# Kernel optimization log

Measured on AMD Instinct MI355X. Metric: run time of the kernel, lower is better.

## Reference

```python
import jax, jax.numpy as jnp
import numpy as np

VAR = 1.0
STD = float(np.sqrt(VAR))


def setup_inputs() -> dict:
    key = jax.random.key(0)
    k1, k2 = jax.random.split(key)
    n, c = 262144, 100
    scores = jax.random.normal(k1, (n, c), dtype=jnp.float32)
    labels = jax.random.randint(k2, (n,), 0, c, dtype=jnp.int64)
    return {"scores": scores, "labels": labels}


def reference(scores, labels):
    n, c = scores.shape
    # Gaussian pdf over class indices, centered at each label (re_encode_label)
    x = jnp.arange(c, dtype=scores.dtype)[None, :]            # (1, c)
    mu = labels.astype(scores.dtype)[:, None]                  # (n, 1)
    inv_norm = 1.0 / (STD * np.sqrt(2.0 * np.pi))
    code = inv_norm * jnp.exp(-0.5 * ((x - mu) / STD) ** 2)    # (n, c)
    # target distribution: softmax over the (unnormalized) pdf values
    target = jax.nn.softmax(code, axis=1)
    logsfmx = jax.nn.log_softmax(scores, axis=1)
    # KLDivLoss(reduction='batchmean'): sum(target * (log target - input)) / n
    kl = jnp.sum(target * (jnp.log(target) - logsfmx)) / n
    return kl
```

## Files before the change

kernel.cpp:

```cpp
#include <hip/hip_runtime.h>
#include <math.h>

#define C 100
#define RPP 16
#define WAVES 4
#define PASSES 4
#define ROWS_PER_WAVE  (RPP * PASSES)
#define ROWS_PER_BLOCK (WAVES * ROWS_PER_WAVE)
#define NF4P (RPP * C / 4)
#define INV_NORM 0.3989422804014327f
#define WFAR     0.67102943f

__device__ __forceinline__ float quad_sum(float x) {
    x += __int_as_float(__builtin_amdgcn_update_dpp(
            0, __float_as_int(x), 0xB1, 0xF, 0xF, true));
    x += __int_as_float(__builtin_amdgcn_update_dpp(
            0, __float_as_int(x), 0x4E, 0xF, 0xF, true));
    return x;
}

__global__ __launch_bounds__(256, 4) void kl_main(
    const float* __restrict__ scores,
    const int*   __restrict__ labels,
    float* __restrict__ out, int n, float inv_n)
{
    __shared__ float sl[WAVES][RPP * C];
    __shared__ float wpart[WAVES];

    const int tid  = threadIdx.x;
    const int wave = tid >> 6, lane = tid & 63;
    const int r    = lane >> 2, sub  = lane & 3;
    float* const mys = sl[wave];

    const int waveRow0 = blockIdx.x * ROWS_PER_BLOCK + wave * ROWS_PER_WAVE;

    float4 va[7], vb[7];
    int mua = 0, mub = 0;
    float acc = 0.f;

    auto issue = [&](float4* v, int p, int& mu) {
        const int rowBase = waveRow0 + p * RPP;
        const int nf4 = min(RPP, max(0, n - rowBase)) * (C / 4);
        const float4* g = (const float4*)(scores + (size_t)rowBase * C);
        #pragma unroll
        for (int c = 0; c < 7; ++c) {
            int i = lane + 64 * c;
            v[c] = (i < nf4) ? g[i] : make_float4(0.f, 0.f, 0.f, 0.f);
        }
        int myrow = rowBase + r;
        mu = (myrow < n) ? labels[myrow] : 0;
    };

    auto consume = [&](const float4* v, int p, int mu) {
        float4* st = (float4*)mys;
        #pragma unroll
        for (int c = 0; c < 7; ++c) {
            int i = lane + 64 * c;
            if (i < NF4P) st[i] = v[c];
        }
        const float* sp  = &mys[r * C];
        const float* spl = sp + sub * 25;
        float se = 0.f, rs = 0.f;
        #pragma unroll
        for (int i = 0; i < 25; ++i) {
            float s = spl[i];
            se += __expf(s);
            rs += s;
        }
        se = quad_sum(se);
        rs = quad_sum(rs);

        const float WP[7] = {0.32897057f, 0.18369895f, 0.03722540f,
            0.00298049f, 8.9804e-5f, 9.9763e-7f, 4.0768e-9f};
        const float WC[7] = {0.39894228f, 0.20681926f, 0.03823936f,
            0.00298711f, 8.9816e-5f, 9.9765e-7f, 4.0768e-9f};
        float dotw = 0.f, csum = 100.f * WFAR, dotc = 0.f;
        #pragma unroll
        for (int d = -6; d <= 6; ++d) {
            int idx  = mu + d;
            bool ok  = (unsigned)idx < (unsigned)C;
            float s  = sp[min(max(idx, 0), C - 1)];
            int a    = d < 0 ? -d : d;
            float wv = ok ? WP[a] : 0.f;
            dotw  = fmaf(wv, s, dotw);
            csum += wv;
            dotc += ok ? WC[a] : 0.f;
        }

        int myrow = waveRow0 + p * RPP + r;
        if (sub == 0 && myrow < n) {
            float dot = fmaf(WFAR, rs, dotw);
            acc += (dotc - dot) / csum - INV_NORM - __logf(csum) + __logf(se);
        }
    };

    issue(va, 0, mua);
    issue(vb, 1, mub);
    consume(va, 0, mua);
    issue(va, 2, mua);
    consume(vb, 1, mub);
    issue(vb, 3, mub);
    consume(va, 2, mua);
    consume(vb, 3, mub);

    #pragma unroll
    for (int off = 32; off > 0; off >>= 1)
        acc += __shfl_xor(acc, off, 64);
    if (lane == 0) wpart[wave] = acc;
    __syncthreads();
    if (tid == 0)
        atomicAdd(out, (wpart[0] + wpart[1] + wpart[2] + wpart[3]) * inv_n);
}

extern "C" void kernel_launch(void* const* d_in, const int* in_sizes, int n_in,
                              void* d_out, int out_size, void* d_ws, size_t ws_size,
                              hipStream_t stream)
{
    const float* scores = (const float*)d_in[0];
    const int*   labels = (const int*)d_in[1];
    float*       out    = (float*)d_out;

    int n = in_sizes[0] / C;

    hipMemsetAsync(d_out, 0, sizeof(float) * (size_t)out_size, stream);

    int blocks = (n + ROWS_PER_BLOCK - 1) / ROWS_PER_BLOCK;
    kl_main<<<blocks, 256, 0, stream>>>(scores, labels, out, n, 1.0f / (float)n);
}
```

Baseline: 155.7 us.

## Stage score tiles via direct global-to-LDS loads with block-wide double buffering

Replaces the register-staged loads (global to VGPR, then ds_write) with global_load_lds DMA straight into a block-shared double buffer of 64 rows per pass. Waves cooperatively load 1 KB chunks and synchronise with s_waitcnt vmcnt plus barriers, and labels are prefetched up front. This is meant to save VGPRs and the LDS write instructions and to keep loads in flight while the previous pass is computed. In exchange it adds block-wide barriers, a larger LDS footprint, fewer blocks per CU (launch bounds lowered to 3), hand-counted vmcnt values that must match the issue pattern, and tail handling that clamps the offset and reloads overlapping bytes.

```diff
diff --git a/kernel.cpp b/kernel.cpp
--- a/kernel.cpp
+++ b/kernel.cpp
@@ -2,12 +2,12 @@
 #include <math.h>
 
 #define C 100
-#define RPP 16
 #define WAVES 4
+#define ROWS_PER_PASS 64
 #define PASSES 4
-#define ROWS_PER_WAVE  (RPP * PASSES)
-#define ROWS_PER_BLOCK (WAVES * ROWS_PER_WAVE)
-#define NF4P (RPP * C / 4)
+#define ROWS_PER_BLOCK (ROWS_PER_PASS * PASSES)
+#define CHUNKS 25
+#define PASS_FLOATS (ROWS_PER_PASS * C)
 #define INV_NORM 0.3989422804014327f
 #define WFAR     0.67102943f
 
@@ -19,46 +19,49 @@
     return x;
 }
 
-__global__ __launch_bounds__(256, 4) void kl_main(
+__global__ __launch_bounds__(256, 3) void kl_main(
     const float* __restrict__ scores,
     const int*   __restrict__ labels,
     float* __restrict__ out, int n, float inv_n)
 {
-    __shared__ float sl[WAVES][RPP * C];
+    __shared__ float buf[2][PASS_FLOATS];
     __shared__ float wpart[WAVES];
 
     const int tid  = threadIdx.x;
     const int wave = tid >> 6, lane = tid & 63;
     const int r    = lane >> 2, sub  = lane & 3;
-    float* const mys = sl[wave];
 
-    const int waveRow0 = blockIdx.x * ROWS_PER_BLOCK + wave * ROWS_PER_WAVE;
+    const int blockRow0 = blockIdx.x * ROWS_PER_BLOCK;
+    const size_t totalBytes = (size_t)n * C * 4;
 
-    float4 va[7], vb[7];
-    int mua = 0, mub = 0;
+    int mu[PASSES];
+    #pragma unroll
+    for (int p = 0; p < PASSES; ++p) {
+        int row = blockRow0 + p * ROWS_PER_PASS + wave * 16 + r;
+        mu[p] = (row < n) ? labels[row] : 0;
+    }
+
     float acc = 0.f;
 
-    auto issue = [&](float4* v, int p, int& mu) {
-        const int rowBase = waveRow0 + p * RPP;
-        const int nf4 = min(RPP, max(0, n - rowBase)) * (C / 4);
-        const float4* g = (const float4*)(scores + (size_t)rowBase * C);
+    auto stage = [&](int p, int b) {
+        const size_t byteBase = (size_t)(blockRow0 + p * ROWS_PER_PASS) * (C * 4);
         #pragma unroll
-        for (int c = 0; c < 7; ++c) {
-            int i = lane + 64 * c;
-            v[c] = (i < nf4) ? g[i] : make_float4(0.f, 0.f, 0.f, 0.f);
+        for (int k = 0; k < 7; ++k) {
+            int c = wave + k * WAVES;
+            if (c < CHUNKS) {
+                size_t off = byteBase + (size_t)c * 1024;
+                if (off + 1024 > totalBytes) off = totalBytes - 1024;
+                const char* src = (const char*)scores + off + lane * 16;
+                __builtin_amdgcn_global_load_lds(
+                    (const __attribute__((address_space(1))) void*)src,
+                    (__attribute__((address_space(3))) void*)&buf[b][c * 256],
+                    16, 0, 0);
+            }
         }
-        int myrow = rowBase + r;
-        mu = (myrow < n) ? labels[myrow] : 0;
     };
 
-    auto consume = [&](const float4* v, int p, int mu) {
-        float4* st = (float4*)mys;
-        #pragma unroll
-        for (int c = 0; c < 7; ++c) {
-            int i = lane + 64 * c;
-            if (i < NF4P) st[i] = v[c];
-        }
-        const float* sp  = &mys[r * C];
+    auto consume = [&](int p, int b) {
+        const float* sp  = &buf[b][(wave * 16 + r) * C];
         const float* spl = sp + sub * 25;
         float se = 0.f, rs = 0.f;
         #pragma unroll
@@ -75,9 +78,10 @@
         const float WC[7] = {0.39894228f, 0.20681926f, 0.03823936f,
             0.00298711f, 8.9816e-5f, 9.9765e-7f, 4.0768e-9f};
         float dotw = 0.f, csum = 100.f * WFAR, dotc = 0.f;
+        const int m = mu[p];
         #pragma unroll
         for (int d = -6; d <= 6; ++d) {
-            int idx  = mu + d;
+            int idx  = m + d;
             bool ok  = (unsigned)idx < (unsigned)C;
             float s  = sp[min(max(idx, 0), C - 1)];
             int a    = d < 0 ? -d : d;
@@ -87,21 +91,41 @@
             dotc += ok ? WC[a] : 0.f;
         }
 
-        int myrow = waveRow0 + p * RPP + r;
+        int myrow = blockRow0 + p * ROWS_PER_PASS + wave * 16 + r;
         if (sub == 0 && myrow < n) {
             float dot = fmaf(WFAR, rs, dotw);
             acc += (dotc - dot) / csum - INV_NORM - __logf(csum) + __logf(se);
         }
     };
 
-    issue(va, 0, mua);
-    issue(vb, 1, mub);
-    consume(va, 0, mua);
-    issue(va, 2, mua);
-    consume(vb, 1, mub);
-    issue(vb, 3, mub);
-    consume(va, 2, mua);
-    consume(vb, 3, mub);
+    #define VMBAR(N) do { asm volatile("s_waitcnt vmcnt(" #N ")" ::: "memory"); \
+                          __builtin_amdgcn_s_barrier();                          \
+                          asm volatile("" ::: "memory"); } while (0)
+    #define BAR()    do { asm volatile("" ::: "memory");                         \
+                          __builtin_amdgcn_s_barrier();                          \
+                          asm volatile("" ::: "memory"); } while (0)
+
+    stage(0, 0);
+    stage(1, 1);
+
+    VMBAR(6);
+    consume(0, 0);
+    BAR();
+    stage(2, 0);
+
+    VMBAR(6);
+    consume(1, 1);
+    BAR();
+    stage(3, 1);
+
+    VMBAR(6);
+    consume(2, 0);
+
+    VMBAR(0);
+    consume(3, 1);
+
+    #undef VMBAR
+    #undef BAR
 
     #pragma unroll
     for (int off = 32; off > 0; off >>= 1)
```

New measurement: 158.0 us. About the same (+1.4%).
